# Kernel tuning notes

Measured on AMD Instinct MI355X. Metric: run time of the kernel, lower is better.

## Reference

```python
import jax, jax.numpy as jnp
import numpy as np
from jax import lax

K_ADA = 0.1
EPS = 1e-5
B, G = 2, 96
C0, C1, C2, C3, F = 1, 16, 32, 64, 64


def adanorm(x, g):
    # AdaNorm over the last (channel) axis: w * (1 - k*xn) * xn
    mean = x.mean(-1, keepdims=True)
    var = ((x - mean) ** 2).mean(-1, keepdims=True) + EPS
    xn = (x - mean) * lax.rsqrt(var)
    return g * (1.0 - K_ADA * xn) * xn


def conv3d(x, w, b, stride):
    # x: [B,D,H,W,Cin], w: [3,3,3,Cin,Cout], padding 1
    y = lax.conv_general_dilated(x, w, (stride,) * 3, [(1, 1)] * 3,
                                 dimension_numbers=('NDHWC', 'DHWIO', 'NDHWC'))
    return y + b


def downsample_mask(m):
    # active output sites of SparseConv3d(k=3, s=2, p=1): any active input in window
    return lax.reduce_window(m, 0.0, lax.max, (1, 3, 3, 3), (1, 2, 2, 2),
                             [(0, 0), (1, 1), (1, 1), (1, 1)])


def setup_inputs() -> dict:
    key = jax.random.key(0)
    ks = jax.random.split(key, 20)
    mask = (jax.random.uniform(ks[0], (B, G, G, G)) < 0.05).astype(jnp.float32)
    x = jax.random.normal(ks[1], (B, G, G, G, C0), jnp.float32) * mask[..., None]

    def wconv(k, cin, cout):
        return jax.random.normal(k, (3, 3, 3, cin, cout), jnp.float32) / np.sqrt(27.0 * cin)

    inp = {'x': x, 'mask': mask}
    chans = [(C0, C1), (C1, C2), (C2, C2), (C2, C3), (C3, C3)]
    for i, (ci, co) in enumerate(chans, start=1):
        inp[f'w{i}'] = wconv(ks[2 * i], ci, co)
        inp[f'b{i}'] = jax.random.normal(ks[2 * i + 1], (co,), jnp.float32) * 0.01
        inp[f'g{i}'] = jnp.ones((co,), jnp.float32)
    inp['wh'] = jax.random.normal(ks[12], (C3, F), jnp.float32) / np.sqrt(C3)
    inp['bh'] = jax.random.normal(ks[13], (F,), jnp.float32) * 0.01
    inp['gh'] = jnp.ones((F,), jnp.float32)
    return inp


def reference(x, mask, w1, b1, g1, w2, b2, g2, w3, b3, g3, w4, b4, g4, w5, b5, g5, wh, bh, gh):
    m1 = mask
    h = conv3d(x, w1, b1, 1) * m1[..., None]            # SubMConv3d
    h = jax.nn.relu(adanorm(h, g1)) * m1[..., None]
    m2 = downsample_mask(m1)
    h = conv3d(h, w2, b2, 2) * m2[..., None]            # SparseConv3d s=2
    h = jax.nn.relu(adanorm(h, g2)) * m2[..., None]
    h = conv3d(h, w3, b3, 1) * m2[..., None]            # SubMConv3d
    h = jax.nn.relu(adanorm(h, g3)) * m2[..., None]
    m3 = downsample_mask(m2)
    h = conv3d(h, w4, b4, 2) * m3[..., None]            # SparseConv3d s=2
    h = jax.nn.relu(adanorm(h, g4)) * m3[..., None]
    h = conv3d(h, w5, b5, 1) * m3[..., None]            # SubMConv3d
    h = jax.nn.relu(adanorm(h, g5)) * m3[..., None]
    # SparseGlobalMaxPool over active voxels
    neg = jnp.asarray(-3.0e38, h.dtype)
    pooled = jnp.where(m3[..., None] > 0, h, neg).max(axis=(1, 2, 3))  # [B, C3]
    # head: Linear -> AdaNorm -> ReLU -> Dropout(eval = identity)
    out = jax.nn.relu(adanorm(pooled @ wh + bh, gh))
    return out
```

## Files before the change

### kernel.cpp

```cpp
#include <hip/hip_runtime.h>
#include <math.h>

#define K_ADA 0.1f
#define NEPS 1e-5f

typedef __attribute__((ext_vector_type(8))) short short8;
typedef __attribute__((ext_vector_type(4))) float f32x4;
typedef unsigned short ushort_t;

__device__ __forceinline__ ushort_t f2b(float f) {
    union { float f; unsigned u; } v; v.f = f;
    unsigned r = (v.u + 0x7fffu + ((v.u >> 16) & 1u)) >> 16;
    return (ushort_t)r;
}

__device__ __forceinline__ float wave_sum64(float v) {
#pragma unroll
    for (int m = 1; m < 64; m <<= 1) v += __shfl_xor(v, m, 64);
    return v;
}

__host__ __device__ constexpr int tapd2(int tap) {
    return tap >= 27 ? 0 : (tap / 9) * 81 + ((tap / 3) % 3) * 9 + (tap % 3);
}

template <int CIN, int COUT>
__device__ __forceinline__ void pack_w_el(const float* __restrict__ w,
                                          ushort_t* __restrict__ wp, int t)
{
    constexpr int NKH = CIN / 32;
    constexpr int NCT = COUT / 16;
    int jj = t & 7;
    int lane = (t >> 3) & 63;
    int rest = t >> 9;
    int kh = rest % NKH;
    int rest2 = rest / NKH;
    int ct = rest2 % NCT;
    int tap = rest2 / NCT;
    int cin = kh * 32 + (lane >> 4) * 8 + jj;
    int cout = ct * 16 + (lane & 15);
    wp[t] = f2b(w[(tap * CIN + cin) * COUT + cout]);
}

__global__ __launch_bounds__(256) void prep_k(
    const float* __restrict__ w1, const float* __restrict__ w2,
    const float* __restrict__ w3, const float* __restrict__ w4,
    const float* __restrict__ w5, const float* __restrict__ m1,
    ushort_t* __restrict__ wp1, ushort_t* __restrict__ wp2,
    ushort_t* __restrict__ wp3, ushort_t* __restrict__ wp4,
    ushort_t* __restrict__ wp5, float* __restrict__ m2,
    float* __restrict__ zeropad, int* __restrict__ counters)
{
    int t = blockIdx.x * 256 + threadIdx.x;
    if (t < 512) {
        int jj = t & 7;
        int lane = t >> 3;
        int tap = (lane >> 4) * 8 + jj;
        int cout = lane & 15;
        wp1[t] = (tap < 27) ? f2b(w1[tap * 16 + cout]) : (ushort_t)0;
    } else if (t < 14848) {
        int u = t - 512;
        int jj = u & 7;
        int lane = (u >> 3) & 63;
        int rest = u >> 9;
        int ct = rest & 1;
        int p = rest >> 1;
        int tap = 2 * p + (lane >> 5);
        int cin = ((lane >> 4) & 1) * 8 + jj;
        int cout = ct * 16 + (lane & 15);
        wp2[u] = (tap < 27) ? f2b(w2[(tap * 16 + cin) * 32 + cout]) : (ushort_t)0;
    } else if (t < 42496) {
        pack_w_el<32, 32>(w3, wp3, t - 14848);
    } else if (t < 97792) {
        pack_w_el<32, 64>(w4, wp4, t - 42496);
    } else if (t < 208384) {
        pack_w_el<64, 64>(w5, wp5, t - 97792);
    } else if (t < 429568) {
        int v = t - 208384;
        constexpr int GO = 48, GI = 96;
        int b = v / (GO * GO * GO);
        int r = v % (GO * GO * GO);
        int d = r / (GO * GO), h = (r / GO) % GO, x = r % GO;
        float mx = 0.f;
        for (int kd = 0; kd < 3; ++kd) {
            int zd = 2 * d + kd - 1; if ((unsigned)zd >= GI) continue;
            for (int kh = 0; kh < 3; ++kh) {
                int zh = 2 * h + kh - 1; if ((unsigned)zh >= GI) continue;
                for (int kw = 0; kw < 3; ++kw) {
                    int zx = 2 * x + kw - 1; if ((unsigned)zx >= GI) continue;
                    mx = fmaxf(mx, m1[((b * GI + zd) * GI + zh) * GI + zx]);
                }
            }
        }
        m2[v] = mx;
    } else if (t < 429576) {
        zeropad[t - 429568] = 0.f;
    } else if (t < 431624) {
        counters[t - 429576] = 0;
    }
}

template <int GO, int GI>
__global__ __launch_bounds__(256) void dmask_k(const float* __restrict__ mi,
                                               float* __restrict__ mo)
{
    constexpr int N = 2 * GO * GO * GO;
    int v = blockIdx.x * 256 + threadIdx.x;
    if (v >= N) return;
    int b = v / (GO * GO * GO);
    int r = v % (GO * GO * GO);
    int d = r / (GO * GO), h = (r / GO) % GO, x = r % GO;
    float mx = 0.f;
    for (int kd = 0; kd < 3; ++kd) {
        int zd = 2 * d + kd - 1; if ((unsigned)zd >= GI) continue;
        for (int kh = 0; kh < 3; ++kh) {
            int zh = 2 * h + kh - 1; if ((unsigned)zh >= GI) continue;
            for (int kw = 0; kw < 3; ++kw) {
                int zx = 2 * x + kw - 1; if ((unsigned)zx >= GI) continue;
                mx = fmaxf(mx, mi[((b * GI + zd) * GI + zh) * GI + zx]);
            }
        }
    }
    mo[v] = mx;
}

__global__ __launch_bounds__(256) void conv1_fill_k(const float* __restrict__ m1,
                                                    ushort_t* __restrict__ h1b,
                                                    int* __restrict__ list,
                                                    int* __restrict__ counters)
{
    int v = blockIdx.x * 256 + threadIdx.x;
    const short8 z = {0, 0, 0, 0, 0, 0, 0, 0};
    short8* hp = reinterpret_cast<short8*>(h1b + (size_t)v * 16);
    hp[0] = z; hp[1] = z;
    bool act = (m1[v] != 0.f);
    unsigned long long msk = __ballot(act);
    int lane = threadIdx.x & 63;
    int gwave = v >> 6;
    int p = gwave & 63;
    int base = 0;
    int cnt = __popcll(msk);
    if (lane == 0 && cnt) base = atomicAdd(&counters[p * 32], cnt);
    base = __shfl(base, 0, 64);
    if (act) {
        int pre = __popcll(msk & ((1ull << lane) - 1ull));
        list[p * 27648 + base + pre] = v;
    }
}

__global__ __launch_bounds__(256) void conv1_act_k(const float* __restrict__ x,
                                                   const int* __restrict__ list,
                                                   const int* __restrict__ counters,
                                                   const ushort_t* __restrict__ wp1,
                                                   const float* __restrict__ bias,
                                                   const float* __restrict__ gain,
                                                   const float* __restrict__ zerof,
                                                   ushort_t* __restrict__ h1b)
{
    constexpr int G = 96, G3 = G * G * G;
    int gwave = (blockIdx.x * 256 + threadIdx.x) >> 6;
    int p = gwave & 63;
    int lw = gwave >> 6;
    int nact = counters[p * 32];
    if (nact <= 0) return;
    const int* plist = list + p * 27648;
    int lane = threadIdx.x & 63;
    int m = lane & 15, q = lane >> 4;
    int nchunk = (nact + 15) >> 4;
    float bn = bias[m], gn = gain[m];
    short8 bfr = *reinterpret_cast<const short8*>(wp1 + lane * 8);

    for (int chunk = lw; chunk < nchunk; chunk += 54) {
        int idx = chunk * 16 + m;
        int vm = plist[min(idx, nact - 1)];
        int b = vm / G3;
        int rr = vm % G3;
        int dm = rr / (G * G), hm = (rr / G) % G, xm = rr % G;

        float xs[8];
#pragma unroll
        for (int j = 0; j < 8; ++j) {
            int k = q * 8 + j;
            int kd = k / 9, kh = (k / 3) % 3, kw = k % 3;
            int id = dm + kd - 1, ih = hm + kh - 1, ix = xm + kw - 1;
            bool ok = (k < 27) && ((unsigned)id < (unsigned)G) &&
                      ((unsigned)ih < (unsigned)G) && ((unsigned)ix < (unsigned)G);
            const float* xp = ok ? (x + (((size_t)b * G + id) * G + ih) * G + ix) : zerof;
            xs[j] = *xp;
        }
        ushort_t av[8];
#pragma unroll
        for (int j = 0; j < 8; ++j) av[j] = f2b(xs[j]);
        short8 a = *reinterpret_cast<short8*>(av);
        f32x4 acc = {0.f, 0.f, 0.f, 0.f};
        acc = __builtin_amdgcn_mfma_f32_16x16x32_bf16(a, bfr, acc, 0, 0, 0);

#pragma unroll
        for (int i = 0; i < 4; ++i) {
            int oidx = chunk * 16 + q * 4 + i;
            float xv = acc[i] + bn;
            float s = xv;
#pragma unroll
            for (int mk = 1; mk < 16; mk <<= 1) s += __shfl_xor(s, mk, 64);
            float mean = s * (1.f / 16.f);
            float dd = xv - mean;
            float ss = dd * dd;
#pragma unroll
            for (int mk = 1; mk < 16; mk <<= 1) ss += __shfl_xor(ss, mk, 64);
            float rs = rsqrtf(ss * (1.f / 16.f) + NEPS);
            float xn = dd * rs;
            float o = fmaxf(gn * (1.f - K_ADA * xn) * xn, 0.f);
            if (oidx < nact) {
                int w = plist[oidx];
                h1b[(size_t)w * 16 + m] = f2b(o);
            }
        }
    }
}

__global__ __launch_bounds__(256, 4) void conv2_tile_k(
    const ushort_t* __restrict__ h1b, const ushort_t* __restrict__ wp2,
    const float* __restrict__ bias, const float* __restrict__ gain,
    const float* __restrict__ m2, const ushort_t* __restrict__ zp,
    ushort_t* __restrict__ h2b)
{
    constexpr int GI = 96, G = 48;
    __shared__ __align__(16) ushort_t halo[729 * 3 * 8];

    int bid = blockIdx.x;
    int b = bid / 1728;
    int r = bid % 1728;
    int td = r / 144, th = (r / 12) % 12, tx = r % 12;
    int d0 = 4 * td, h0 = 4 * th, x0 = 4 * tx;
    int bd = 2 * d0 - 1, bh = 2 * h0 - 1, bx = 2 * x0 - 1;

    for (int c = threadIdx.x; c < 1458; c += 256) {
        int hv = c >> 1, j = c & 1;
        int gd = bd + hv / 81;
        int gh = bh + (hv / 9) % 9;
        int gx = bx + hv % 9;
        bool ok = ((unsigned)gd < (unsigned)GI) && ((unsigned)gh < (unsigned)GI) &&
                  ((unsigned)gx < (unsigned)GI);
        const ushort_t* p = ok ? (h1b + ((((size_t)b * GI + gd) * GI + gh) * GI + gx) * 16 + j * 8) : zp;
        *reinterpret_cast<short8*>(halo + ((size_t)hv * 3 + j) * 8) =
            *reinterpret_cast<const short8*>(p);
    }
    __syncthreads();

    int wv = threadIdx.x >> 6;
    int lane = threadIdx.x & 63;
    int m = lane & 15, q = lane >> 4;
    int mh = m >> 2, mx = m & 3;
    int tq = q >> 1, hq = q & 1;
    int hbase = 162 * wv + 18 * mh + 2 * mx;

    f32x4 accs[2];
#pragma unroll
    for (int ct = 0; ct < 2; ++ct) {
        f32x4 acc = {0.f, 0.f, 0.f, 0.f};
#pragma unroll
        for (int g = 0; g < 2; ++g) {
            short8 ab[7], bb[7];
#pragma unroll
            for (int j = 0; j < 7; ++j) {
                const int p = g * 7 + j;
                int hv = hbase + (tq ? tapd2(2 * p + 1) : tapd2(2 * p));
                ab[j] = *reinterpret_cast<const short8*>(halo + ((size_t)hv * 3 + hq) * 8);
                bb[j] = *reinterpret_cast<const short8*>(
                    wp2 + ((size_t)(p * 2 + ct) * 64 + lane) * 8);
            }
#pragma unroll
            for (int j = 0; j < 7; ++j)
                acc = __builtin_amdgcn_mfma_f32_16x16x32_bf16(ab[j], bb[j], acc, 0, 0, 0);
        }
        accs[ct] = acc;
    }

    float b0 = bias[m], b1 = bias[16 + m];
    float g0 = gain[m], g1 = gain[16 + m];
#pragma unroll
    for (int i = 0; i < 4; ++i) {
        int rr2 = q * 4 + i;
        int w = ((b * G + d0 + wv) * G + h0 + (rr2 >> 2)) * G + x0 + (rr2 & 3);
        float xv0 = accs[0][i] + b0;
        float xv1 = accs[1][i] + b1;
        float s = xv0 + xv1;
#pragma unroll
        for (int mk = 1; mk < 16; mk <<= 1) s += __shfl_xor(s, mk, 64);
        float mean = s * (1.f / 32.f);
        float dd0 = xv0 - mean, dd1 = xv1 - mean;
        float ss = dd0 * dd0 + dd1 * dd1;
#pragma unroll
        for (int mk = 1; mk < 16; mk <<= 1) ss += __shfl_xor(ss, mk, 64);
        float rs = rsqrtf(ss * (1.f / 32.f) + NEPS);
        float mv = m2[w];
        float xn0 = dd0 * rs, xn1 = dd1 * rs;
        float o0 = fmaxf(g0 * (1.f - K_ADA * xn0) * xn0, 0.f);
        float o1 = fmaxf(g1 * (1.f - K_ADA * xn1) * xn1, 0.f);
        if (mv == 0.f) { o0 = 0.f; o1 = 0.f; }
        h2b[(size_t)w * 32 + m]      = f2b(o0);
        h2b[(size_t)w * 32 + 16 + m] = f2b(o1);
    }
}

__global__ __launch_bounds__(256, 4) void conv3_tile_k(
    const ushort_t* __restrict__ h2b, const ushort_t* __restrict__ wp3,
    const float* __restrict__ bias, const float* __restrict__ gain,
    const float* __restrict__ m2, const ushort_t* __restrict__ zp,
    ushort_t* __restrict__ h3b)
{
    constexpr int G = 48;
    __shared__ __align__(16) ushort_t halo[216 * 5 * 8];

    int bid = blockIdx.x;
    int b = bid / 1728;
    int r = bid % 1728;
    int td = r / 144, th = (r / 12) % 12, tx = r % 12;
    int d0 = 4 * td, h0 = 4 * th, x0 = 4 * tx;
    int bd = d0 - 1, bh = h0 - 1, bx = x0 - 1;

    for (int c = threadIdx.x; c < 864; c += 256) {
        int hv = c >> 2, j = c & 3;
        int gd = bd + hv / 36;
        int gh = bh + (hv / 6) % 6;
        int gx = bx + hv % 6;
        bool ok = ((unsigned)gd < (unsigned)G) && ((unsigned)gh < (unsigned)G) &&
                  ((unsigned)gx < (unsigned)G);
        const ushort_t* p = ok ? (h2b + ((((size_t)b * G + gd) * G + gh) * G + gx) * 32 + j * 8) : zp;
        *reinterpret_cast<short8*>(halo + ((size_t)hv * 5 + j) * 8) =
            *reinterpret_cast<const short8*>(p);
    }
    __syncthreads();

    int wv = threadIdx.x >> 6;
    int lane = threadIdx.x & 63;
    int m = lane & 15, q = lane >> 4;
    int mh = m >> 2, mx = m & 3;
    int hbase = 36 * wv + 6 * mh + mx;

    f32x4 accs[2];
#pragma unroll
    for (int ct = 0; ct < 2; ++ct) {
        f32x4 acc = {0.f, 0.f, 0.f, 0.f};
#pragma unroll
        for (int g = 0; g < 3; ++g) {
            short8 ab[9], bb[9];
#pragma unroll
            for (int j = 0; j < 9; ++j) {
                const int tap = g * 9 + j;
                const int kd = tap / 9, kh = (tap / 3) % 3, kw = tap % 3;
                int hv = hbase + kd * 36 + kh * 6 + kw;
                ab[j] = *reinterpret_cast<const short8*>(halo + ((size_t)hv * 5 + q) * 8);
                bb[j] = *reinterpret_cast<const short8*>(
                    wp3 + ((size_t)(tap * 2 + ct) * 64 + lane) * 8);
            }
#pragma unroll
            for (int j = 0; j < 9; ++j)
                acc = __builtin_amdgcn_mfma_f32_16x16x32_bf16(ab[j], bb[j], acc, 0, 0, 0);
        }
        accs[ct] = acc;
    }

    float b0 = bias[m], b1 = bias[16 + m];
    float g0 = gain[m], g1 = gain[16 + m];
#pragma unroll
    for (int i = 0; i < 4; ++i) {
        int rr2 = q * 4 + i;
        int w = ((b * G + d0 + wv) * G + h0 + (rr2 >> 2)) * G + x0 + (rr2 & 3);
        float xv0 = accs[0][i] + b0;
        float xv1 = accs[1][i] + b1;
        float s = xv0 + xv1;
#pragma unroll
        for (int mk = 1; mk < 16; mk <<= 1) s += __shfl_xor(s, mk, 64);
        float mean = s * (1.f / 32.f);
        float dd0 = xv0 - mean, dd1 = xv1 - mean;
        float ss = dd0 * dd0 + dd1 * dd1;
#pragma unroll
        for (int mk = 1; mk < 16; mk <<= 1) ss += __shfl_xor(ss, mk, 64);
        float rs = rsqrtf(ss * (1.f / 32.f) + NEPS);
        float mv = m2[w];
        float xn0 = dd0 * rs, xn1 = dd1 * rs;
        float o0 = fmaxf(g0 * (1.f - K_ADA * xn0) * xn0, 0.f);
        float o1 = fmaxf(g1 * (1.f - K_ADA * xn1) * xn1, 0.f);
        if (mv == 0.f) { o0 = 0.f; o1 = 0.f; }
        h3b[(size_t)w * 32 + m]      = f2b(o0);
        h3b[(size_t)w * 32 + 16 + m] = f2b(o1);
    }
}

template <int G_IN, int CIN, int STRIDE, bool OUTB>
__global__ __launch_bounds__(256, 4) void conv45_tile_k(
    const ushort_t* __restrict__ Ab, const ushort_t* __restrict__ Wp,
    const float* __restrict__ bias, const float* __restrict__ gain,
    const float* __restrict__ mask,
    ushort_t* __restrict__ outb, float* __restrict__ outf)
{
    constexpr int G = 24;
    constexpr int NKH = CIN / 32;
    constexpr int NCH = CIN / 8;
    constexpr int PADC = NCH + 1;
    constexpr int HD = STRIDE + 3;
    constexpr int HH = STRIDE + 3;
    constexpr int HX = 3 * STRIDE + 3;
    constexpr int NHV = HD * HH * HX;
    constexpr int NCHUNK = NHV * NCH;

    __shared__ __align__(16) ushort_t halo[NHV * PADC * 8];
    __shared__ float nbuf[16][65];

    int bid = blockIdx.x;
    int b = bid / 864;
    int r = bid % 864;
    int td = r / 72, th = (r / 6) % 12, tx = r % 6;
    int d0 = 2 * td, h0 = 2 * th, x0 = 4 * tx;
    int bd = d0 * STRIDE - 1, bh = h0 * STRIDE - 1, bx = x0 * STRIDE - 1;

    for (int c = threadIdx.x; c < NCHUNK; c += 256) {
        int hv = c / NCH, j = c % NCH;
        int gd = bd + hv / (HH * HX);
        int gh = bh + (hv / HX) % HH;
        int gx = bx + hv % HX;
        short8 val = {0, 0, 0, 0, 0, 0, 0, 0};
        if ((unsigned)gd < (unsigned)G_IN && (unsigned)gh < (unsigned)G_IN &&
            (unsigned)gx < (unsigned)G_IN)
            val = *reinterpret_cast<const short8*>(
                Ab + ((((size_t)b * G_IN + gd) * G_IN + gh) * G_IN + gx) * CIN + j * 8);
        *reinterpret_cast<short8*>(halo + ((size_t)hv * PADC + j) * 8) = val;
    }
    __syncthreads();

    int ct = threadIdx.x >> 6;
    int lane = threadIdx.x & 63;
    int m = lane & 15, q = lane >> 4;
    int md = (m >> 3) & 1, mh = (m >> 2) & 1, mx = m & 3;

    f32x4 acc = {0.f, 0.f, 0.f, 0.f};
    constexpr int NT = 27 * NKH;
    constexpr int GSZ = 9;
#pragma unroll
    for (int g = 0; g < NT / GSZ; ++g) {
        short8 ab[GSZ], bb[GSZ];
#pragma unroll
        for (int j = 0; j < GSZ; ++j) {
            int it = g * GSZ + j;
            int tap = it / NKH, k2 = it % NKH;
            const int kd = tap / 9, kh = (tap / 3) % 3, kw = tap % 3;
            int hv = ((md * STRIDE + kd) * HH + (mh * STRIDE + kh)) * HX +
                     (mx * STRIDE + kw);
            ab[j] = *reinterpret_cast<const short8*>(
                halo + ((size_t)hv * PADC + k2 * 4 + q) * 8);
            bb[j] = *reinterpret_cast<const short8*>(
                Wp + (((size_t)(tap * 4 + ct) * NKH + k2) * 64 + lane) * 8);
        }
#pragma unroll
        for (int j = 0; j < GSZ; ++j)
            acc = __builtin_amdgcn_mfma_f32_16x16x32_bf16(ab[j], bb[j], acc, 0, 0, 0);
    }

    float bn = bias[ct * 16 + m];
#pragma unroll
    for (int i = 0; i < 4; ++i) nbuf[q * 4 + i][ct * 16 + m] = acc[i] + bn;
    __syncthreads();

    float gn = gain[lane];
#pragma unroll
    for (int i = 0; i < 4; ++i) {
        int vloc = ct * 4 + i;
        int vd = d0 + ((vloc >> 3) & 1);
        int vh = h0 + ((vloc >> 2) & 1);
        int vx = x0 + (vloc & 3);
        int w = ((b * G + vd) * G + vh) * G + vx;
        float val = nbuf[vloc][lane];
        float mean = wave_sum64(val) * (1.f / 64.f);
        float dd = val - mean;
        float var = wave_sum64(dd * dd) * (1.f / 64.f) + NEPS;
        float xn = dd * rsqrtf(var);
        float o = fmaxf(gn * (1.f - K_ADA * xn) * xn, 0.f);
        if (mask[w] == 0.f) o = 0.f;
        if (OUTB) outb[(size_t)w * 64 + lane] = f2b(o);
        else      outf[(size_t)w * 64 + lane] = o;
    }
}

__global__ __launch_bounds__(256) void pool1_k(const float* __restrict__ h5,
                                               float* __restrict__ partials)
{
    int chunk = blockIdx.x % 54;
    int b = blockIdx.x / 54;
    int c = threadIdx.x & 63;
    int s = threadIdx.x >> 6;
    const float* base = h5 + ((size_t)b * 13824 + chunk * 256) * 64;
    float mx = 0.f;
#pragma unroll 4
    for (int v = s; v < 256; v += 4) mx = fmaxf(mx, base[v * 64 + c]);
    __shared__ float red[256];
    red[threadIdx.x] = mx;
    __syncthreads();
    if (s == 0)
        partials[blockIdx.x * 64 + c] =
            fmaxf(fmaxf(red[c], red[64 + c]), fmaxf(red[128 + c], red[192 + c]));
}

__global__ __launch_bounds__(128) void pool2_head_k(const float* __restrict__ partials,
                                                    const float* __restrict__ wh,
                                                    const float* __restrict__ bh,
                                                    const float* __restrict__ gh,
                                                    float* __restrict__ out)
{
    __shared__ float pooled[2][64];
    int t = threadIdx.x;
    int b = t >> 6;
    int f = t & 63;
    float mx = 0.f;
    for (int p = 0; p < 54; ++p) mx = fmaxf(mx, partials[(b * 54 + p) * 64 + f]);
    pooled[b][f] = mx;
    __syncthreads();
    float acc = bh[f];
#pragma unroll
    for (int k = 0; k < 64; ++k) acc += pooled[b][k] * wh[k * 64 + f];
    float mean = wave_sum64(acc) * (1.f / 64.f);
    float dd = acc - mean;
    float var = wave_sum64(dd * dd) * (1.f / 64.f) + NEPS;
    float xn = dd * rsqrtf(var);
    float val = gh[f] * (1.f - K_ADA * xn) * xn;
    out[t] = fmaxf(val, 0.f);
}

extern "C" void kernel_launch(void* const* d_in, const int* in_sizes, int n_in,
                              void* d_out, int out_size, void* d_ws, size_t ws_size,
                              hipStream_t stream)
{
    const float* x  = (const float*)d_in[0];
    const float* m1 = (const float*)d_in[1];
    const float* w1 = (const float*)d_in[2];
    const float* b1 = (const float*)d_in[3];
    const float* g1 = (const float*)d_in[4];
    const float* w2 = (const float*)d_in[5];
    const float* b2 = (const float*)d_in[6];
    const float* g2 = (const float*)d_in[7];
    const float* w3 = (const float*)d_in[8];
    const float* b3 = (const float*)d_in[9];
    const float* g3 = (const float*)d_in[10];
    const float* w4 = (const float*)d_in[11];
    const float* b4 = (const float*)d_in[12];
    const float* g4 = (const float*)d_in[13];
    const float* w5 = (const float*)d_in[14];
    const float* b5 = (const float*)d_in[15];
    const float* g5 = (const float*)d_in[16];
    const float* wh = (const float*)d_in[17];
    const float* bh = (const float*)d_in[18];
    const float* gh = (const float*)d_in[19];
    float* out = (float*)d_out;

    float* ws = (float*)d_ws;
    ushort_t* h1b = (ushort_t*)ws;
    ushort_t* h2b = (ushort_t*)(ws + 14155776);
    ushort_t* h3b = (ushort_t*)(ws + 17694720);
    ushort_t* h4b = (ushort_t*)(ws + 21233664);
    float* h5 = ws + 22118400;
    float* m2 = ws + 23887872;
    float* m3 = ws + 24109056;
    float* partials = ws + 24136704;
    ushort_t* wp1 = (ushort_t*)(ws + 24143616);
    ushort_t* wp2 = (ushort_t*)(ws + 24143872);
    ushort_t* wp3 = (ushort_t*)(ws + 24151040);
    ushort_t* wp4 = (ushort_t*)(ws + 24164864);
    ushort_t* wp5 = (ushort_t*)(ws + 24192512);
    float* zeropad = ws + 24247808;
    int* counters = (int*)(ws + 24247816);
    int* list = (int*)(ws + 14155776);

    prep_k<<<1687, 256, 0, stream>>>(w1, w2, w3, w4, w5, m1,
                                     wp1, wp2, wp3, wp4, wp5, m2, zeropad, counters);
    dmask_k<24, 48><<<108, 256, 0, stream>>>(m2, m3);

    const ushort_t* zp = (const ushort_t*)zeropad;
    conv1_fill_k<<<6912, 256, 0, stream>>>(m1, h1b, list, counters);
    conv1_act_k<<<864, 256, 0, stream>>>(x, list, counters, wp1, b1, g1, zeropad, h1b);
    conv2_tile_k<<<3456, 256, 0, stream>>>(h1b, wp2, b2, g2, m2, zp, h2b);
    conv3_tile_k<<<3456, 256, 0, stream>>>(h2b, wp3, b3, g3, m2, zp, h3b);
    conv45_tile_k<48, 32, 2, true><<<1728, 256, 0, stream>>>(h3b, wp4, b4, g4, m3, h4b, nullptr);
    conv45_tile_k<24, 64, 1, false><<<1728, 256, 0, stream>>>(h4b, wp5, b5, g5, m3, nullptr, h5);

    pool1_k<<<108, 256, 0, stream>>>(h5, partials);
    pool2_head_k<<<1, 128, 0, stream>>>(partials, wh, bh, gh, out);
}
```

Before: 244.1 us.

## Fuse global max-pool into conv5 epilogue; restructure conv2/conv3 MFMA work split

Conv5 no longer writes its fp32 activation buffer. Each block reduces its per-channel maximum and merges it into a zeroed pooled buffer with an atomicMax on the float bits, which removes the pool1 kernel and its pass over a large buffer. Conv2 now reuses each A fragment for both output-channel tiles, and conv3 splits its waves by channel tile and spatial pair, then normalises through a shared-memory transpose. The conv3 occupancy hint drops from 4 to 3, and the float-as-uint atomicMax is only correct because the post-ReLU values are non-negative.

```diff
diff --git a/kernel.cpp b/kernel.cpp
--- a/kernel.cpp
+++ b/kernel.cpp
@@ -49,7 +49,8 @@
     ushort_t* __restrict__ wp1, ushort_t* __restrict__ wp2,
     ushort_t* __restrict__ wp3, ushort_t* __restrict__ wp4,
     ushort_t* __restrict__ wp5, float* __restrict__ m2,
-    float* __restrict__ zeropad, int* __restrict__ counters)
+    float* __restrict__ zeropad, int* __restrict__ counters,
+    float* __restrict__ pooled)
 {
     int t = blockIdx.x * 256 + threadIdx.x;
     if (t < 512) {
@@ -97,6 +98,8 @@
         zeropad[t - 429568] = 0.f;
     } else if (t < 431624) {
         counters[t - 429576] = 0;
+    } else if (t < 431752) {
+        pooled[t - 431624] = 0.f;
     }
 }
 
@@ -254,36 +257,33 @@
     int tq = q >> 1, hq = q & 1;
     int hbase = 162 * wv + 18 * mh + 2 * mx;
 
-    f32x4 accs[2];
-#pragma unroll
-    for (int ct = 0; ct < 2; ++ct) {
-        f32x4 acc = {0.f, 0.f, 0.f, 0.f};
-#pragma unroll
-        for (int g = 0; g < 2; ++g) {
-            short8 ab[7], bb[7];
-#pragma unroll
-            for (int j = 0; j < 7; ++j) {
-                const int p = g * 7 + j;
-                int hv = hbase + (tq ? tapd2(2 * p + 1) : tapd2(2 * p));
-                ab[j] = *reinterpret_cast<const short8*>(halo + ((size_t)hv * 3 + hq) * 8);
-                bb[j] = *reinterpret_cast<const short8*>(
-                    wp2 + ((size_t)(p * 2 + ct) * 64 + lane) * 8);
-            }
-#pragma unroll
-            for (int j = 0; j < 7; ++j)
-                acc = __builtin_amdgcn_mfma_f32_16x16x32_bf16(ab[j], bb[j], acc, 0, 0, 0);
-        }
-        accs[ct] = acc;
-    }
-
-    float b0 = bias[m], b1 = bias[16 + m];
-    float g0 = gain[m], g1 = gain[16 + m];
+    f32x4 acc0 = {0.f, 0.f, 0.f, 0.f}, acc1 = acc0;
+#pragma unroll
+    for (int g = 0; g < 2; ++g) {
+        short8 a[7], b0[7], b1[7];
+#pragma unroll
+        for (int j = 0; j < 7; ++j) {
+            const int p = g * 7 + j;
+            int hv = hbase + (tq ? tapd2(2 * p + 1) : tapd2(2 * p));
+            a[j] = *reinterpret_cast<const short8*>(halo + ((size_t)hv * 3 + hq) * 8);
+            b0[j] = *reinterpret_cast<const short8*>(wp2 + ((size_t)(p * 2 + 0) * 64 + lane) * 8);
+            b1[j] = *reinterpret_cast<const short8*>(wp2 + ((size_t)(p * 2 + 1) * 64 + lane) * 8);
+        }
+#pragma unroll
+        for (int j = 0; j < 7; ++j) {
+            acc0 = __builtin_amdgcn_mfma_f32_16x16x32_bf16(a[j], b0[j], acc0, 0, 0, 0);
+            acc1 = __builtin_amdgcn_mfma_f32_16x16x32_bf16(a[j], b1[j], acc1, 0, 0, 0);
+        }
+    }
+
+    float b0s = bias[m], b1s = bias[16 + m];
+    float g0s = gain[m], g1s = gain[16 + m];
 #pragma unroll
     for (int i = 0; i < 4; ++i) {
         int rr2 = q * 4 + i;
         int w = ((b * G + d0 + wv) * G + h0 + (rr2 >> 2)) * G + x0 + (rr2 & 3);
-        float xv0 = accs[0][i] + b0;
-        float xv1 = accs[1][i] + b1;
+        float xv0 = acc0[i] + b0s;
+        float xv1 = acc1[i] + b1s;
         float s = xv0 + xv1;
 #pragma unroll
         for (int mk = 1; mk < 16; mk <<= 1) s += __shfl_xor(s, mk, 64);
@@ -295,15 +295,15 @@
         float rs = rsqrtf(ss * (1.f / 32.f) + NEPS);
         float mv = m2[w];
         float xn0 = dd0 * rs, xn1 = dd1 * rs;
-        float o0 = fmaxf(g0 * (1.f - K_ADA * xn0) * xn0, 0.f);
-        float o1 = fmaxf(g1 * (1.f - K_ADA * xn1) * xn1, 0.f);
+        float o0 = fmaxf(g0s * (1.f - K_ADA * xn0) * xn0, 0.f);
+        float o1 = fmaxf(g1s * (1.f - K_ADA * xn1) * xn1, 0.f);
         if (mv == 0.f) { o0 = 0.f; o1 = 0.f; }
         h2b[(size_t)w * 32 + m]      = f2b(o0);
         h2b[(size_t)w * 32 + 16 + m] = f2b(o1);
     }
 }
 
-__global__ __launch_bounds__(256, 4) void conv3_tile_k(
+__global__ __launch_bounds__(256, 3) void conv3_tile_k(
     const ushort_t* __restrict__ h2b, const ushort_t* __restrict__ wp3,
     const float* __restrict__ bias, const float* __restrict__ gain,
     const float* __restrict__ m2, const ushort_t* __restrict__ zp,
@@ -311,6 +311,7 @@
 {
     constexpr int G = 48;
     __shared__ __align__(16) ushort_t halo[216 * 5 * 8];
+    __shared__ float nbuf[64][33];
 
     int bid = blockIdx.x;
     int b = bid / 1728;
@@ -336,64 +337,72 @@
     int lane = threadIdx.x & 63;
     int m = lane & 15, q = lane >> 4;
     int mh = m >> 2, mx = m & 3;
-    int hbase = 36 * wv + 6 * mh + mx;
-
-    f32x4 accs[2];
-#pragma unroll
-    for (int ct = 0; ct < 2; ++ct) {
-        f32x4 acc = {0.f, 0.f, 0.f, 0.f};
-#pragma unroll
-        for (int g = 0; g < 3; ++g) {
-            short8 ab[9], bb[9];
-#pragma unroll
-            for (int j = 0; j < 9; ++j) {
-                const int tap = g * 9 + j;
-                const int kd = tap / 9, kh = (tap / 3) % 3, kw = tap % 3;
-                int hv = hbase + kd * 36 + kh * 6 + kw;
-                ab[j] = *reinterpret_cast<const short8*>(halo + ((size_t)hv * 5 + q) * 8);
-                bb[j] = *reinterpret_cast<const short8*>(
-                    wp3 + ((size_t)(tap * 2 + ct) * 64 + lane) * 8);
-            }
-#pragma unroll
-            for (int j = 0; j < 9; ++j)
-                acc = __builtin_amdgcn_mfma_f32_16x16x32_bf16(ab[j], bb[j], acc, 0, 0, 0);
-        }
-        accs[ct] = acc;
-    }
-
-    float b0 = bias[m], b1 = bias[16 + m];
-    float g0 = gain[m], g1 = gain[16 + m];
+    int ct = wv & 1;
+    int sp = wv >> 1;
+    int hb0 = 36 * (2 * sp) + 6 * mh + mx;
+    int hb1 = hb0 + 36;
+
+    f32x4 acc0 = {0.f, 0.f, 0.f, 0.f}, acc1 = acc0;
+#pragma unroll
+    for (int g = 0; g < 3; ++g) {
+        short8 a0[9], a1[9], bb[9];
+#pragma unroll
+        for (int j = 0; j < 9; ++j) {
+            const int tap = g * 9 + j;
+            const int dlt = (tap / 9) * 36 + ((tap / 3) % 3) * 6 + (tap % 3);
+            a0[j] = *reinterpret_cast<const short8*>(halo + ((size_t)(hb0 + dlt) * 5 + q) * 8);
+            a1[j] = *reinterpret_cast<const short8*>(halo + ((size_t)(hb1 + dlt) * 5 + q) * 8);
+            bb[j] = *reinterpret_cast<const short8*>(
+                wp3 + ((size_t)(tap * 2 + ct) * 64 + lane) * 8);
+        }
+#pragma unroll
+        for (int j = 0; j < 9; ++j) {
+            acc0 = __builtin_amdgcn_mfma_f32_16x16x32_bf16(a0[j], bb[j], acc0, 0, 0, 0);
+            acc1 = __builtin_amdgcn_mfma_f32_16x16x32_bf16(a1[j], bb[j], acc1, 0, 0, 0);
+        }
+    }
+
+    float bn = bias[ct * 16 + m];
 #pragma unroll
     for (int i = 0; i < 4; ++i) {
         int rr2 = q * 4 + i;
-        int w = ((b * G + d0 + wv) * G + h0 + (rr2 >> 2)) * G + x0 + (rr2 & 3);
-        float xv0 = accs[0][i] + b0;
-        float xv1 = accs[1][i] + b1;
-        float s = xv0 + xv1;
-#pragma unroll
-        for (int mk = 1; mk < 16; mk <<= 1) s += __shfl_xor(s, mk, 64);
+        nbuf[(2 * sp) * 16 + rr2][ct * 16 + m]     = acc0[i] + bn;
+        nbuf[(2 * sp + 1) * 16 + rr2][ct * 16 + m] = acc1[i] + bn;
+    }
+    __syncthreads();
+
+    int hh = lane >> 5;
+    int ch = lane & 31;
+    float gns = gain[ch];
+    float bswap; (void)bswap;
+#pragma unroll
+    for (int it = 0; it < 8; ++it) {
+        int vloc = wv * 16 + it * 2 + hh;
+        float val = nbuf[vloc][ch];
+        float s = val;
+#pragma unroll
+        for (int mk = 1; mk < 32; mk <<= 1) s += __shfl_xor(s, mk, 64);
         float mean = s * (1.f / 32.f);
-        float dd0 = xv0 - mean, dd1 = xv1 - mean;
-        float ss = dd0 * dd0 + dd1 * dd1;
-#pragma unroll
-        for (int mk = 1; mk < 16; mk <<= 1) ss += __shfl_xor(ss, mk, 64);
+        float dd = val - mean;
+        float ss = dd * dd;
+#pragma unroll
+        for (int mk = 1; mk < 32; mk <<= 1) ss += __shfl_xor(ss, mk, 64);
         float rs = rsqrtf(ss * (1.f / 32.f) + NEPS);
-        float mv = m2[w];
-        float xn0 = dd0 * rs, xn1 = dd1 * rs;
-        float o0 = fmaxf(g0 * (1.f - K_ADA * xn0) * xn0, 0.f);
-        float o1 = fmaxf(g1 * (1.f - K_ADA * xn1) * xn1, 0.f);
-        if (mv == 0.f) { o0 = 0.f; o1 = 0.f; }
-        h3b[(size_t)w * 32 + m]      = f2b(o0);
-        h3b[(size_t)w * 32 + 16 + m] = f2b(o1);
-    }
-}
-
-template <int G_IN, int CIN, int STRIDE, bool OUTB>
+        int slice = vloc >> 4, rr2 = vloc & 15;
+        int w = ((b * G + d0 + slice) * G + h0 + (rr2 >> 2)) * G + x0 + (rr2 & 3);
+        float xn = dd * rs;
+        float o = fmaxf(gns * (1.f - K_ADA * xn) * xn, 0.f);
+        if (m2[w] == 0.f) o = 0.f;
+        h3b[(size_t)w * 32 + ch] = f2b(o);
+    }
+}
+
+template <int G_IN, int CIN, int STRIDE, bool POOL>
 __global__ __launch_bounds__(256, 4) void conv45_tile_k(
     const ushort_t* __restrict__ Ab, const ushort_t* __restrict__ Wp,
     const float* __restrict__ bias, const float* __restrict__ gain,
     const float* __restrict__ mask,
-    ushort_t* __restrict__ outb, float* __restrict__ outf)
+    ushort_t* __restrict__ outb, unsigned* __restrict__ pooled)
 {
     constexpr int G = 24;
     constexpr int NKH = CIN / 32;
@@ -407,6 +416,7 @@
 
     __shared__ __align__(16) ushort_t halo[NHV * PADC * 8];
     __shared__ float nbuf[16][65];
+    __shared__ float pbuf[4][64];
 
     int bid = blockIdx.x;
     int b = bid / 864;
@@ -463,6 +473,7 @@
     __syncthreads();
 
     float gn = gain[lane];
+    float wavemax = 0.f;
 #pragma unroll
     for (int i = 0; i < 4; ++i) {
         int vloc = ct * 4 + i;
@@ -477,47 +488,35 @@
         float xn = dd * rsqrtf(var);
         float o = fmaxf(gn * (1.f - K_ADA * xn) * xn, 0.f);
         if (mask[w] == 0.f) o = 0.f;
-        if (OUTB) outb[(size_t)w * 64 + lane] = f2b(o);
-        else      outf[(size_t)w * 64 + lane] = o;
-    }
-}
-
-__global__ __launch_bounds__(256) void pool1_k(const float* __restrict__ h5,
-                                               float* __restrict__ partials)
-{
-    int chunk = blockIdx.x % 54;
-    int b = blockIdx.x / 54;
-    int c = threadIdx.x & 63;
-    int s = threadIdx.x >> 6;
-    const float* base = h5 + ((size_t)b * 13824 + chunk * 256) * 64;
-    float mx = 0.f;
-#pragma unroll 4
-    for (int v = s; v < 256; v += 4) mx = fmaxf(mx, base[v * 64 + c]);
-    __shared__ float red[256];
-    red[threadIdx.x] = mx;
-    __syncthreads();
-    if (s == 0)
-        partials[blockIdx.x * 64 + c] =
-            fmaxf(fmaxf(red[c], red[64 + c]), fmaxf(red[128 + c], red[192 + c]));
-}
-
-__global__ __launch_bounds__(128) void pool2_head_k(const float* __restrict__ partials,
-                                                    const float* __restrict__ wh,
-                                                    const float* __restrict__ bh,
-                                                    const float* __restrict__ gh,
-                                                    float* __restrict__ out)
-{
-    __shared__ float pooled[2][64];
+        if (POOL) wavemax = fmaxf(wavemax, o);
+        else      outb[(size_t)w * 64 + lane] = f2b(o);
+    }
+    if (POOL) {
+        pbuf[ct][lane] = wavemax;
+        __syncthreads();
+        if (ct == 0) {
+            float v = fmaxf(fmaxf(pbuf[0][lane], pbuf[1][lane]),
+                            fmaxf(pbuf[2][lane], pbuf[3][lane]));
+            atomicMax(&pooled[b * 64 + lane], __float_as_uint(v));
+        }
+    }
+}
+
+__global__ __launch_bounds__(128) void head_k(const float* __restrict__ pooled,
+                                              const float* __restrict__ wh,
+                                              const float* __restrict__ bh,
+                                              const float* __restrict__ gh,
+                                              float* __restrict__ out)
+{
+    __shared__ float pl[2][64];
     int t = threadIdx.x;
     int b = t >> 6;
     int f = t & 63;
-    float mx = 0.f;
-    for (int p = 0; p < 54; ++p) mx = fmaxf(mx, partials[(b * 54 + p) * 64 + f]);
-    pooled[b][f] = mx;
+    pl[b][f] = pooled[b * 64 + f];
     __syncthreads();
     float acc = bh[f];
 #pragma unroll
-    for (int k = 0; k < 64; ++k) acc += pooled[b][k] * wh[k * 64 + f];
+    for (int k = 0; k < 64; ++k) acc += pl[b][k] * wh[k * 64 + f];
     float mean = wave_sum64(acc) * (1.f / 64.f);
     float dd = acc - mean;
     float var = wave_sum64(dd * dd) * (1.f / 64.f) + NEPS;
@@ -557,21 +556,21 @@
     ushort_t* h2b = (ushort_t*)(ws + 14155776);
     ushort_t* h3b = (ushort_t*)(ws + 17694720);
     ushort_t* h4b = (ushort_t*)(ws + 21233664);
-    float* h5 = ws + 22118400;
-    float* m2 = ws + 23887872;
-    float* m3 = ws + 24109056;
-    float* partials = ws + 24136704;
-    ushort_t* wp1 = (ushort_t*)(ws + 24143616);
-    ushort_t* wp2 = (ushort_t*)(ws + 24143872);
-    ushort_t* wp3 = (ushort_t*)(ws + 24151040);
-    ushort_t* wp4 = (ushort_t*)(ws + 24164864);
-    ushort_t* wp5 = (ushort_t*)(ws + 24192512);
-    float* zeropad = ws + 24247808;
-    int* counters = (int*)(ws + 24247816);
+    float* m2 = ws + 22118400;
+    float* m3 = ws + 22339584;
+    ushort_t* wp1 = (ushort_t*)(ws + 22367232);
+    ushort_t* wp2 = (ushort_t*)(ws + 22367488);
+    ushort_t* wp3 = (ushort_t*)(ws + 22374656);
+    ushort_t* wp4 = (ushort_t*)(ws + 22388480);
+    ushort_t* wp5 = (ushort_t*)(ws + 22416128);
+    float* zeropad = ws + 22471424;
+    int* counters = (int*)(ws + 22471432);
+    float* pooled = ws + 22473480;
     int* list = (int*)(ws + 14155776);
 
     prep_k<<<1687, 256, 0, stream>>>(w1, w2, w3, w4, w5, m1,
-                                     wp1, wp2, wp3, wp4, wp5, m2, zeropad, counters);
+                                     wp1, wp2, wp3, wp4, wp5, m2, zeropad,
+                                     counters, pooled);
     dmask_k<24, 48><<<108, 256, 0, stream>>>(m2, m3);
 
     const ushort_t* zp = (const ushort_t*)zeropad;
@@ -579,9 +578,8 @@
     conv1_act_k<<<864, 256, 0, stream>>>(x, list, counters, wp1, b1, g1, zeropad, h1b);
     conv2_tile_k<<<3456, 256, 0, stream>>>(h1b, wp2, b2, g2, m2, zp, h2b);
     conv3_tile_k<<<3456, 256, 0, stream>>>(h2b, wp3, b3, g3, m2, zp, h3b);
-    conv45_tile_k<48, 32, 2, true><<<1728, 256, 0, stream>>>(h3b, wp4, b4, g4, m3, h4b, nullptr);
-    conv45_tile_k<24, 64, 1, false><<<1728, 256, 0, stream>>>(h4b, wp5, b5, g5, m3, nullptr, h5);
-
-    pool1_k<<<108, 256, 0, stream>>>(h5, partials);
-    pool2_head_k<<<1, 128, 0, stream>>>(partials, wh, bh, gh, out);
-}
+    conv45_tile_k<48, 32, 2, false><<<1728, 256, 0, stream>>>(h3b, wp4, b4, g4, m3, h4b, nullptr);
+    conv45_tile_k<24, 64, 1, true><<<1728, 256, 0, stream>>>(h4b, wp5, b5, g5, m3, nullptr,
+                                                             (unsigned*)pooled);
+    head_k<<<1, 128, 0, stream>>>(pooled, wh, bh, gh, out);
+}
```

Result: faster. 237.1 us (-2.9%).
